# Kernel optimization log

Measured on AMD Instinct MI355X. Metric: run time of the kernel, lower is better.

The kernel has to match this reference:

```python
import jax, jax.numpy as jnp
import numpy as np

B, T, D_IN, D_SAE, K, KS = 32, 16, 768, 16384, 32, 3


def setup_inputs() -> dict:
    key = jax.random.key(0)
    k1, k2, k3 = jax.random.split(key, 3)
    x = jax.random.normal(k1, (B, T, D_IN), dtype=jnp.float32)
    # Conv1d weight (out_ch=d_sae, in_ch=d_in, kernel), scaled by 1/sqrt(d_in*kernel)
    conv_w = jax.random.normal(k2, (D_SAE, D_IN, KS), dtype=jnp.float32) * (1.0 / np.sqrt(D_IN * KS))
    b_enc = jnp.zeros((D_SAE,), dtype=jnp.float32)
    W_dec = jax.random.normal(k3, (D_SAE, T, D_IN), dtype=jnp.float32) * (1.0 / np.sqrt(D_SAE))
    b_dec = jnp.zeros((T, D_IN), dtype=jnp.float32)
    return {"x": x, "conv_w": conv_w, "b_enc": b_enc, "W_dec": W_dec, "b_dec": b_dec}


def reference(x, conv_w, b_enc, W_dec, b_dec):
    # encode: shared 1-D conv across T, 'same' padding, no bias
    h = jax.lax.conv_general_dilated(
        jnp.transpose(x, (0, 2, 1)),           # (B, d_in, T)
        conv_w,                                 # (d_sae, d_in, KS)
        window_strides=(1,),
        padding=[(KS // 2, KS // 2)],
        dimension_numbers=("NCH", "OIH", "NCH"),
    )                                           # (B, d_sae, T)
    pre = jnp.sum(h, axis=-1) + b_enc           # pool='sum' -> (B, d_sae)
    # TopK sparsify: keep relu of the k largest preactivations per row
    vals, idx = jax.lax.top_k(pre, K)           # (B, K)
    rows = jnp.arange(pre.shape[0])[:, None]
    z = jnp.zeros_like(pre).at[rows, idx].set(jax.nn.relu(vals))
    # decode: dense einsum over all d_sae features
    x_hat = jnp.einsum("bs,std->btd", z, W_dec) + b_dec
    recon_loss = jnp.mean(jnp.sum((x_hat - x) ** 2, axis=-1))
    return recon_loss, x_hat, z
```

## Files before the change

kernel.cpp:

```cpp
#include <hip/hip_runtime.h>
#include <hip/hip_bf16.h>
#include <float.h>

#define DIN   768
#define DSAE  16384
#define K_    32
#define CAND  64
#define KTOT  2304
#define TD    12288
#define KSPLIT 4
#define NCHT  72
#define NCH   18

typedef __attribute__((ext_vector_type(8))) short bf16x8;
typedef __attribute__((ext_vector_type(4))) float f32x4;

__device__ __forceinline__ short f2bf(float f) {
    unsigned u = __float_as_uint(f);
    u += 0x7FFFu + ((u >> 16) & 1u);
    return (short)(u >> 16);
}

__global__ __launch_bounds__(256) void prep_kernel(const float* __restrict__ x,
                                                   float* __restrict__ A_T,
                                                   short* __restrict__ frag) {
    int g = blockIdx.x * 256 + threadIdx.x;
    int b = g / DIN;
    int d = g - b * DIN;
    const float* xp = x + (size_t)b * TD + d;
    float S = 0.f;
    float x0 = xp[0];
    float xl = xp[15 * DIN];
    #pragma unroll
    for (int t = 0; t < 16; ++t) S += xp[t * DIN];
    float v0 = S - xl, v1 = S, v2 = S - x0;
    int base = d * 96 + b;
    A_T[base]      = v0;
    A_T[base + 32] = v1;
    A_T[base + 64] = v2;
    const int h = b >> 4, bl = b & 15;
    #pragma unroll
    for (int j = 0; j < 3; ++j) {
        int k = 3 * d + j;
        float val = (j == 0) ? v0 : (j == 1) ? v1 : v2;
        int c = k >> 5, kk = k & 31;
        size_t idx = (((size_t)(c * 2 + h) * 64) + (((kk >> 3) << 4) | bl)) * 8 + (kk & 7);
        frag[idx] = f2bf(val);
    }
}

__global__ __launch_bounds__(256, 4) void enc_mfma_kernel(
    const float* __restrict__ W,
    const short* __restrict__ frag,
    float* __restrict__ partial)
{
    const int tid  = threadIdx.x;
    const int bid  = blockIdx.x;
    const int ks   = bid & 3;
    const int l    = tid & 63;
    const int w    = tid >> 6;
    const int strip = (bid >> 2) * 4 + w;
    const int s0    = strip << 4;
    const int row   = s0 + (l & 15);
    const int klane = (l >> 4) << 3;

    const float* wrow = W + (size_t)row * KTOT;

    f32x4 acc0 = {0.f, 0.f, 0.f, 0.f};
    f32x4 acc1 = {0.f, 0.f, 0.f, 0.f};

    #pragma unroll 2
    for (int ch = 0; ch < NCH; ++ch) {
        const int cg = ks * NCH + ch;
        const int kb = (cg << 5) + klane;
        const float4 wa = *(const float4*)&wrow[kb];
        const float4 wb = *(const float4*)&wrow[kb + 4];
        bf16x8 wf;
        wf[0] = f2bf(wa.x); wf[1] = f2bf(wa.y); wf[2] = f2bf(wa.z); wf[3] = f2bf(wa.w);
        wf[4] = f2bf(wb.x); wf[5] = f2bf(wb.y); wf[6] = f2bf(wb.z); wf[7] = f2bf(wb.w);
        const bf16x8 a0 = *(const bf16x8*)&frag[((size_t)(cg * 2    ) * 64 + l) * 8];
        const bf16x8 a1 = *(const bf16x8*)&frag[((size_t)(cg * 2 + 1) * 64 + l) * 8];
        acc0 = __builtin_amdgcn_mfma_f32_16x16x32_bf16(wf, a0, acc0, 0, 0, 0);
        acc1 = __builtin_amdgcn_mfma_f32_16x16x32_bf16(wf, a1, acc1, 0, 0, 0);
    }

    const int bcol  = l & 15;
    const int sbase = s0 + ((l >> 4) << 2);
    float* p0 = partial + ((size_t)(ks * 32) + bcol) * DSAE + sbase;
    float* p1 = p0 + (size_t)16 * DSAE;
    #pragma unroll
    for (int r = 0; r < 4; ++r) { p0[r] = acc0[r]; p1[r] = acc1[r]; }
}

__global__ __launch_bounds__(256) void combine_kernel(const float* __restrict__ partial,
                                                      const float* __restrict__ b_enc,
                                                      float* __restrict__ pre,
                                                      float* __restrict__ out0) {
    int g  = blockIdx.x * 256 + threadIdx.x;
    int b  = g >> 12;
    int s4 = g & 4095;
    const float4* p = (const float4*)partial;
    float4 acc = p[(size_t)b * 4096 + s4];
    #pragma unroll
    for (int ks = 1; ks < KSPLIT; ++ks) {
        float4 v = p[(size_t)(ks * 32 + b) * 4096 + s4];
        acc.x += v.x; acc.y += v.y; acc.z += v.z; acc.w += v.w;
    }
    float4 be = ((const float4*)b_enc)[s4];
    acc.x += be.x; acc.y += be.y; acc.z += be.z; acc.w += be.w;
    ((float4*)pre)[(size_t)b * 4096 + s4] = acc;
    if (g == 0) *out0 = 0.f;
}

__global__ __launch_bounds__(1024, 1) void topk_kernel(
    float* __restrict__ z,
    const float* __restrict__ A_T,
    const float* __restrict__ W,
    const float* __restrict__ b_enc,
    float* __restrict__ sel_val,
    int*   __restrict__ sel_idx)
{
    __shared__ unsigned hist[256];
    __shared__ unsigned gsfx[65];
    __shared__ unsigned sfx[257];
    __shared__ int      sdelta;
    __shared__ unsigned scnt;
    __shared__ int      l_idx[CAND];
    __shared__ float    ex_val[CAND];
    __shared__ int      rnk[CAND];
    __shared__ int      eq_min;
    __shared__ float    A_col[KTOT];

    const int t = threadIdx.x;
    const int b = blockIdx.x;
    float* zrow = z + (size_t)b * DSAE;

    unsigned u[16];
    #pragma unroll
    for (int i = 0; i < 16; ++i) {
        unsigned xb = __float_as_uint(zrow[t + (i << 10)]);
        u[i] = (xb & 0x80000000u) ? ~xb : (xb | 0x80000000u);
    }

    unsigned prefix = 0, pmask = 0;
    int need = CAND;
    for (int p = 0; p < 4; ++p) {
        const int shift = 24 - 8 * p;
        if (t < 256) hist[t] = 0;
        __syncthreads();
        #pragma unroll
        for (int i = 0; i < 16; ++i)
            if ((u[i] & pmask) == prefix)
                atomicAdd(&hist[(u[i] >> shift) & 255u], 1u);
        __syncthreads();
        if (t < 64) {
            unsigned s4 = hist[4*t] + hist[4*t+1] + hist[4*t+2] + hist[4*t+3];
            #pragma unroll
            for (int off = 1; off < 64; off <<= 1) {
                unsigned o = __shfl_down(s4, off, 64);
                if (t + off < 64) s4 += o;
            }
            gsfx[t] = s4;
            if (t == 0) gsfx[64] = 0;
        }
        __syncthreads();
        if (t < 256) {
            int q = t >> 2;
            unsigned acc = gsfx[q + 1];
            for (int d = 4*q + 3; d >= t; --d) acc += hist[d];
            sfx[t] = acc;
            if (t == 0) sfx[256] = 0;
        }
        __syncthreads();
        if (t < 256) {
            if (sfx[t] >= (unsigned)need && sfx[t + 1] < (unsigned)need) sdelta = t;
        }
        __syncthreads();
        const int dlt = sdelta;
        need  -= (int)sfx[dlt + 1];
        prefix |= ((unsigned)dlt) << shift;
        pmask  |= 0xFFu << shift;
        __syncthreads();
    }

    const unsigned ustar = prefix;
    if (t == 0) scnt = 0;
    __syncthreads();
    unsigned eqmask = 0;
    #pragma unroll
    for (int i = 0; i < 16; ++i) {
        int idx = t + (i << 10);
        if (u[i] > ustar) {
            unsigned s = atomicAdd(&scnt, 1u);
            l_idx[s] = idx;
        } else if (u[i] == ustar) {
            eqmask |= (1u << i);
        }
    }
    __syncthreads();
    const int needf = need;
    for (int r = 0; r < needf; ++r) {
        if (t == 0) eq_min = 0x7FFFFFFF;
        __syncthreads();
        #pragma unroll
        for (int i = 0; i < 16; ++i)
            if (eqmask & (1u << i)) atomicMin(&eq_min, t + (i << 10));
        __syncthreads();
        #pragma unroll
        for (int i = 0; i < 16; ++i)
            if ((eqmask & (1u << i)) && (t + (i << 10) == eq_min)) {
                eqmask &= ~(1u << i);
                unsigned s = atomicAdd(&scnt, 1u);
                l_idx[s] = eq_min;
            }
        __syncthreads();
    }

    for (int q = t; q < KTOT; q += 1024) A_col[q] = A_T[q * 32 + b];
    __syncthreads();

    {
        const int j = t >> 4, t16 = t & 15;
        const int cand = l_idx[j];
        const float* wr = W + (size_t)cand * KTOT;
        float s = 0.f;
        for (int q = t16; q < 576; q += 16) {
            const float4 wv = *(const float4*)&wr[q << 2];
            const int k4 = q << 2;
            s += wv.x * A_col[k4] + wv.y * A_col[k4 + 1]
               + wv.z * A_col[k4 + 2] + wv.w * A_col[k4 + 3];
        }
        s += __shfl_xor(s, 1, 64);
        s += __shfl_xor(s, 2, 64);
        s += __shfl_xor(s, 4, 64);
        s += __shfl_xor(s, 8, 64);
        if (t16 == 0) ex_val[j] = s + b_enc[cand];
    }
    __syncthreads();

    if (t < CAND) {
        float v = ex_val[t]; int ix = l_idx[t];
        int r = 0;
        for (int j2 = 0; j2 < CAND; ++j2) {
            float v2 = ex_val[j2]; int ix2 = l_idx[j2];
            r += (v2 > v || (v2 == v && ix2 < ix)) ? 1 : 0;
        }
        rnk[t] = r;
    }
    __syncthreads();
    #pragma unroll
    for (int i = 0; i < 16; ++i) zrow[t + (i << 10)] = 0.f;
    __syncthreads();
    if (t < CAND && rnk[t] < K_) {
        int ix = l_idx[t];
        float v = ex_val[t];
        int pos = 0;
        for (int j2 = 0; j2 < CAND; ++j2)
            pos += (rnk[j2] < K_ && l_idx[j2] < ix) ? 1 : 0;
        float val = v > 0.f ? v : 0.f;
        zrow[ix] = val;
        sel_val[(b << 5) + pos] = val;
        sel_idx[(b << 5) + pos] = ix;
    }
}

__global__ __launch_bounds__(256, 4) void decode_kernel(
    const float* __restrict__ W_dec,
    const float* __restrict__ b_dec,
    const float* __restrict__ x,
    const float* __restrict__ sel_val,
    const int*   __restrict__ sel_idx,
    float* __restrict__ xhat,
    float* __restrict__ out0)
{
    __shared__ float sv[K_];
    __shared__ int   si[K_];
    __shared__ float wsum[4];

    const int t     = threadIdx.x;
    const int blk   = blockIdx.x;
    const int b     = blk / 12;
    const int chunk = blk - b * 12;

    if (t < K_) { sv[t] = sel_val[(b << 5) + t]; si[t] = sel_idx[(b << 5) + t]; }
    __syncthreads();

    const int e = chunk * 1024 + t * 4;
    float4 acc = *(const float4*)&b_dec[e];
    #pragma unroll 8
    for (int j = 0; j < K_; ++j) {
        const float val = sv[j];
        const float4 wd = *(const float4*)&W_dec[(size_t)si[j] * TD + e];
        acc.x += val * wd.x;
        acc.y += val * wd.y;
        acc.z += val * wd.z;
        acc.w += val * wd.w;
    }

    const size_t xo = (size_t)b * TD + e;
    xhat[xo + 0] = acc.x;
    xhat[xo + 1] = acc.y;
    xhat[xo + 2] = acc.z;
    xhat[xo + 3] = acc.w;

    const float4 xv = *(const float4*)&x[xo];
    float dx = acc.x - xv.x, dy = acc.y - xv.y;
    float dz = acc.z - xv.z, dw = acc.w - xv.w;
    float ss = dx * dx + dy * dy + dz * dz + dw * dw;
    #pragma unroll
    for (int off = 32; off > 0; off >>= 1) ss += __shfl_down(ss, off, 64);
    if ((t & 63) == 0) wsum[t >> 6] = ss;
    __syncthreads();
    if (t == 0)
        atomicAdd(out0, (wsum[0] + wsum[1] + wsum[2] + wsum[3]) * (1.0f / 512.0f));
}

extern "C" void kernel_launch(void* const* d_in, const int* in_sizes, int n_in,
                              void* d_out, int out_size, void* d_ws, size_t ws_size,
                              hipStream_t stream) {
    const float* x      = (const float*)d_in[0];
    const float* conv_w = (const float*)d_in[1];
    const float* b_enc  = (const float*)d_in[2];
    const float* W_dec  = (const float*)d_in[3];
    const float* b_dec  = (const float*)d_in[4];

    float* out  = (float*)d_out;
    float* xhat = out + 1;
    float* z    = out + 1 + 393216;

    float* partial_enc = (float*)d_ws;
    float* A_T         = (float*)((char*)d_ws + (12u << 20));
    short* frag        = (short*)((char*)d_ws + (13u << 20));
    float* sel_val     = (float*)((char*)d_ws + (14u << 20));
    int*   sel_idx     = (int*)  ((char*)d_ws + (14u << 20) + 4096);

    prep_kernel    <<<96,   256,  0, stream>>>(x, A_T, frag);
    enc_mfma_kernel<<<1024, 256,  0, stream>>>(conv_w, frag, partial_enc);
    combine_kernel <<<512,  256,  0, stream>>>(partial_enc, b_enc, z, out);
    topk_kernel    <<<32,   1024, 0, stream>>>(z, A_T, conv_w, b_enc, sel_val, sel_idx);
    decode_kernel  <<<384,  256,  0, stream>>>(W_dec, b_dec, x, sel_val, sel_idx, xhat, out);
}
```

Before: 87.62 us.

## Fuse split-K combine into top-k, halve K split, parallelize prep over time

Removes the separate combine kernel by having the top-k kernel sum the split-K partials and bias directly when loading each row. The encoder's K split drops from four to two, halving the partial buffer traffic but doubling per-block loop length with half as many blocks. The prep kernel now uses four threads per (b,d) pair with shuffles to form the time sums, and zeroes the loss output in place of the removed combine kernel. The z row is no longer written by combine, so top-k must write it itself elsewhere (presumably already does for final z).

```diff
diff --git a/kernel.cpp b/kernel.cpp
--- a/kernel.cpp
+++ b/kernel.cpp
@@ -8,9 +8,8 @@
 #define CAND  64
 #define KTOT  2304
 #define TD    12288
-#define KSPLIT 4
-#define NCHT  72
-#define NCH   18
+#define KSPLIT 2
+#define NCH   36
 
 typedef __attribute__((ext_vector_type(8))) short bf16x8;
 typedef __attribute__((ext_vector_type(4))) float f32x4;
@@ -21,32 +20,49 @@
     return (short)(u >> 16);
 }
 
+__device__ __forceinline__ void frag_store(short* frag, int k, int b, float val) {
+    int c = k >> 5, kk = k & 31;
+    size_t idx = (((size_t)(c * 2 + (b >> 4)) * 64) + (((kk >> 3) << 4) | (b & 15))) * 8
+               + (kk & 7);
+    frag[idx] = f2bf(val);
+}
+
 __global__ __launch_bounds__(256) void prep_kernel(const float* __restrict__ x,
                                                    float* __restrict__ A_T,
-                                                   short* __restrict__ frag) {
+                                                   short* __restrict__ frag,
+                                                   float* __restrict__ out0) {
     int g = blockIdx.x * 256 + threadIdx.x;
-    int b = g / DIN;
-    int d = g - b * DIN;
+    int pair = g >> 2, q = g & 3;
+    int b = pair / DIN;
+    int d = pair - b * DIN;
     const float* xp = x + (size_t)b * TD + d;
-    float S = 0.f;
-    float x0 = xp[0];
-    float xl = xp[15 * DIN];
-    #pragma unroll
-    for (int t = 0; t < 16; ++t) S += xp[t * DIN];
-    float v0 = S - xl, v1 = S, v2 = S - x0;
+
+    float v0 = xp[(4 * q + 0) * DIN];
+    float v1 = xp[(4 * q + 1) * DIN];
+    float v2 = xp[(4 * q + 2) * DIN];
+    float v3 = xp[(4 * q + 3) * DIN];
+    float S = v0 + v1 + v2 + v3;
+    S += __shfl_xor(S, 1, 64);
+    S += __shfl_xor(S, 2, 64);
+    float xf = __shfl_xor(v0, 1, 64);
+    float xl = __shfl_xor(v3, 1, 64);
+
     int base = d * 96 + b;
-    A_T[base]      = v0;
-    A_T[base + 32] = v1;
-    A_T[base + 64] = v2;
-    const int h = b >> 4, bl = b & 15;
-    #pragma unroll
-    for (int j = 0; j < 3; ++j) {
-        int k = 3 * d + j;
-        float val = (j == 0) ? v0 : (j == 1) ? v1 : v2;
-        int c = k >> 5, kk = k & 31;
-        size_t idx = (((size_t)(c * 2 + h) * 64) + (((kk >> 3) << 4) | bl)) * 8 + (kk & 7);
-        frag[idx] = f2bf(val);
-    }
+    int k0 = 3 * d;
+    if (q == 0) {
+        A_T[base + 32] = S;
+    } else if (q == 1) {
+        float u2 = S - xf;
+        A_T[base + 64] = u2;
+        frag_store(frag, k0 + 2, b, u2);
+    } else if (q == 2) {
+        float u0 = S - xl;
+        A_T[base] = u0;
+        frag_store(frag, k0, b, u0);
+    } else {
+        frag_store(frag, k0 + 1, b, S);
+    }
+    if (g == 0) *out0 = 0.f;
 }
 
 __global__ __launch_bounds__(256, 4) void enc_mfma_kernel(
@@ -56,10 +72,10 @@
 {
     const int tid  = threadIdx.x;
     const int bid  = blockIdx.x;
-    const int ks   = bid & 3;
+    const int ks   = bid & 1;
     const int l    = tid & 63;
     const int w    = tid >> 6;
-    const int strip = (bid >> 2) * 4 + w;
+    const int strip = (bid >> 1) * 4 + w;
     const int s0    = strip << 4;
     const int row   = s0 + (l & 15);
     const int klane = (l >> 4) << 3;
@@ -92,31 +108,12 @@
     for (int r = 0; r < 4; ++r) { p0[r] = acc0[r]; p1[r] = acc1[r]; }
 }
 
-__global__ __launch_bounds__(256) void combine_kernel(const float* __restrict__ partial,
-                                                      const float* __restrict__ b_enc,
-                                                      float* __restrict__ pre,
-                                                      float* __restrict__ out0) {
-    int g  = blockIdx.x * 256 + threadIdx.x;
-    int b  = g >> 12;
-    int s4 = g & 4095;
-    const float4* p = (const float4*)partial;
-    float4 acc = p[(size_t)b * 4096 + s4];
-    #pragma unroll
-    for (int ks = 1; ks < KSPLIT; ++ks) {
-        float4 v = p[(size_t)(ks * 32 + b) * 4096 + s4];
-        acc.x += v.x; acc.y += v.y; acc.z += v.z; acc.w += v.w;
-    }
-    float4 be = ((const float4*)b_enc)[s4];
-    acc.x += be.x; acc.y += be.y; acc.z += be.z; acc.w += be.w;
-    ((float4*)pre)[(size_t)b * 4096 + s4] = acc;
-    if (g == 0) *out0 = 0.f;
-}
-
 __global__ __launch_bounds__(1024, 1) void topk_kernel(
+    const float* __restrict__ partial,
+    const float* __restrict__ b_enc,
     float* __restrict__ z,
     const float* __restrict__ A_T,
     const float* __restrict__ W,
-    const float* __restrict__ b_enc,
     float* __restrict__ sel_val,
     int*   __restrict__ sel_idx)
 {
@@ -138,7 +135,11 @@
     unsigned u[16];
     #pragma unroll
     for (int i = 0; i < 16; ++i) {
-        unsigned xb = __float_as_uint(zrow[t + (i << 10)]);
+        const int col = t + (i << 10);
+        float f = b_enc[col]
+                + partial[(size_t)b * DSAE + col]
+                + partial[(size_t)(32 + b) * DSAE + col];
+        unsigned xb = __float_as_uint(f);
         u[i] = (xb & 0x80000000u) ? ~xb : (xb | 0x80000000u);
     }
 
@@ -329,14 +330,14 @@
     float* z    = out + 1 + 393216;
 
     float* partial_enc = (float*)d_ws;
-    float* A_T         = (float*)((char*)d_ws + (12u << 20));
-    short* frag        = (short*)((char*)d_ws + (13u << 20));
-    float* sel_val     = (float*)((char*)d_ws + (14u << 20));
-    int*   sel_idx     = (int*)  ((char*)d_ws + (14u << 20) + 4096);
-
-    prep_kernel    <<<96,   256,  0, stream>>>(x, A_T, frag);
-    enc_mfma_kernel<<<1024, 256,  0, stream>>>(conv_w, frag, partial_enc);
-    combine_kernel <<<512,  256,  0, stream>>>(partial_enc, b_enc, z, out);
-    topk_kernel    <<<32,   1024, 0, stream>>>(z, A_T, conv_w, b_enc, sel_val, sel_idx);
-    decode_kernel  <<<384,  256,  0, stream>>>(W_dec, b_dec, x, sel_val, sel_idx, xhat, out);
-}
+    float* A_T         = (float*)((char*)d_ws + (6u << 20));
+    short* frag        = (short*)((char*)d_ws + (7u << 20));
+    float* sel_val     = (float*)((char*)d_ws + (8u << 20));
+    int*   sel_idx     = (int*)  ((char*)d_ws + (8u << 20) + 4096);
+
+    prep_kernel    <<<384, 256,  0, stream>>>(x, A_T, frag, out);
+    enc_mfma_kernel<<<512, 256,  0, stream>>>(conv_w, frag, partial_enc);
+    topk_kernel    <<<32,  1024, 0, stream>>>(partial_enc, b_enc, z, A_T, conv_w,
+                                              sel_val, sel_idx);
+    decode_kernel  <<<384, 256,  0, stream>>>(W_dec, b_dec, x, sel_val, sel_idx, xhat, out);
+}
```

Result: faster. 83.00 us (median of 2 runs) (-5.3%).
